# Kernel tuning notes

Hardware: AMD Instinct MI355X
Metric: run time of the kernel (lower is better)

The kernel has to match this reference:

```python
import jax, jax.numpy as jnp
import numpy as np

N = 10000          # num nodes
E = 640000         # num edges (avg degree 64)
IN_CH = 128
OUT_CH = 128


def setup_inputs() -> dict:
    key = jax.random.key(0)
    k_x, k_ei, k_ea, k_w1, k_b1, k_w2, k_b2 = jax.random.split(key, 7)
    x = jax.random.normal(k_x, (N, IN_CH), dtype=jnp.float32)
    edge_index = jax.random.randint(k_ei, (2, E), 0, N, dtype=jnp.int64)
    edge_attr = jax.random.uniform(k_ea, (E,), dtype=jnp.float32)
    # MLP params: Linear(2*in, out) -> ReLU -> Linear(out, out), stored as [in, out]
    s1 = 1.0 / np.sqrt(2 * IN_CH)
    s2 = 1.0 / np.sqrt(OUT_CH)
    W1 = jax.random.uniform(k_w1, (2 * IN_CH, OUT_CH), jnp.float32, -s1, s1)
    b1 = jax.random.uniform(k_b1, (OUT_CH,), jnp.float32, -s1, s1)
    W2 = jax.random.uniform(k_w2, (OUT_CH, OUT_CH), jnp.float32, -s2, s2)
    b2 = jax.random.uniform(k_b2, (OUT_CH,), jnp.float32, -s2, s2)
    return {"x": x, "edge_index": edge_index, "edge_attr": edge_attr,
            "W1": W1, "b1": b1, "W2": W2, "b2": b2}


def reference(x, edge_index, edge_attr, W1, b1, W2, b2):
    row, col = edge_index[0], edge_index[1]
    # message: scale sender feature by edge_attr, concat with receiver feature, 2-layer MLP
    x_i = x[row] * edge_attr[:, None]          # [E, in]
    x_j = x[col]                               # [E, in]
    combined = jnp.concatenate([x_i, x_j], axis=1)  # [E, 2*in]
    h = jax.nn.relu(combined @ W1 + b1)        # [E, out]
    messages = h @ W2 + b2                     # [E, out]
    # sum aggregation: scatter-add messages into receiving nodes (col)
    out = jnp.zeros((x.shape[0], messages.shape[1]), dtype=messages.dtype)
    out = out.at[col].add(messages)
    return out
```

## Files before the change

kernel.cpp:

```cpp
#include <hip/hip_runtime.h>

#define C 128
#define NPB 16
#define CAP 128
#define OVF_MAX 65536
#define CSTRIDE 16
#define EPT 8

__device__ __forceinline__ unsigned bf16_bits(float x) {
    unsigned u = __float_as_uint(x);
    u += 0x7FFFu + ((u >> 16) & 1u);
    return u >> 16;
}
__device__ __forceinline__ float bf16f(unsigned short b) {
    return __uint_as_float(((unsigned)b) << 16);
}

__global__ void fused_pre_kernel(const float* __restrict__ x, const float* __restrict__ W1,
                                 unsigned short* __restrict__ P16, float* __restrict__ Q,
                                 const int* __restrict__ ei, const float* __restrict__ attr,
                                 int* __restrict__ cursor, int* __restrict__ ovf_cnt,
                                 int2* __restrict__ ovf, unsigned* __restrict__ sorted,
                                 int N, int E, int SB) {
    if ((int)blockIdx.x < SB) {
        const int base = (blockIdx.x * 256 + threadIdx.x) * EPT;
        if (base >= E) return;
        if (base + EPT <= E) {
            const int4 r0 = *(const int4*)(ei + base);
            const int4 r1 = *(const int4*)(ei + base + 4);
            const int4 c0 = *(const int4*)(ei + (size_t)E + base);
            const int4 c1 = *(const int4*)(ei + (size_t)E + base + 4);
            const float4 a0 = *(const float4*)(attr + base);
            const float4 a1 = *(const float4*)(attr + base + 4);
            const int rows[EPT] = {r0.x, r0.y, r0.z, r0.w, r1.x, r1.y, r1.z, r1.w};
            const int cols[EPT] = {c0.x, c0.y, c0.z, c0.w, c1.x, c1.y, c1.z, c1.w};
            const float as[EPT] = {a0.x, a0.y, a0.z, a0.w, a1.x, a1.y, a1.z, a1.w};
            int pos[EPT];
#pragma unroll
            for (int j = 0; j < EPT; ++j)
                pos[j] = atomicAdd(&cursor[cols[j] * CSTRIDE], 1);
#pragma unroll
            for (int j = 0; j < EPT; ++j) {
                const unsigned v = (bf16_bits(as[j]) << 16) | (unsigned)rows[j];
                if (pos[j] < CAP) {
                    sorted[(size_t)cols[j] * CAP + pos[j]] = v;
                } else {
                    const int o = atomicAdd(ovf_cnt, 1);
                    if (o < OVF_MAX) ovf[o] = make_int2(cols[j], (int)v);
                }
            }
        } else {
            for (int e = base; e < E; ++e) {
                const int row = ei[e], colv = ei[(size_t)E + e];
                const int pos = atomicAdd(&cursor[colv * CSTRIDE], 1);
                const unsigned v = (bf16_bits(attr[e]) << 16) | (unsigned)row;
                if (pos < CAP) sorted[(size_t)colv * CAP + pos] = v;
                else {
                    const int o = atomicAdd(ovf_cnt, 1);
                    if (o < OVF_MAX) ovf[o] = make_int2(colv, (int)v);
                }
            }
        }
    } else {
        __shared__ float xs[NPB][C];
        const int pb = blockIdx.x - SB;
        const int n0 = pb * NPB;
        const int tt = threadIdx.x & (C - 1);
        const int half = threadIdx.x >> 7;
        for (int i = threadIdx.x; i < NPB * C; i += 256) {
            const int gi = n0 * C + i;
            xs[0][i] = (gi < N * C) ? x[gi] : 0.f;
        }
        __syncthreads();
        const float* __restrict__ Wb = W1 + (half ? (C * C) : 0) + tt;
        float acc[NPB] = {};
        for (int k = 0; k < C; ++k) {
            const float w = Wb[k * C];
#pragma unroll
            for (int j = 0; j < NPB; ++j)
                acc[j] = fmaf(xs[j][k], w, acc[j]);
        }
#pragma unroll
        for (int j = 0; j < NPB; ++j)
            if (n0 + j < N) {
                if (half) Q[(size_t)(n0 + j) * C + tt] = acc[j];
                else      P16[(size_t)(n0 + j) * C + tt] = (unsigned short)bf16_bits(acc[j]);
            }
    }
}

__global__ void agg_out_kernel(const unsigned* __restrict__ sorted, const int* __restrict__ cursor,
                               const unsigned short* __restrict__ P16, const float* __restrict__ Q,
                               const float* __restrict__ b1, const float* __restrict__ W2,
                               const float* __restrict__ b2,
                               const int* __restrict__ ovf_cnt, const int2* __restrict__ ovf,
                               float* __restrict__ out, int N) {
    __shared__ float4 part[2][4][32];
    __shared__ float hs[2][C];
    const int t = threadIdx.x;
    const int j = t >> 7;
    const int slice = (t >> 5) & 3;
    const int ch4 = t & 31;
    const int n = blockIdx.x * 2 + j;

    float4 acc = make_float4(0.f, 0.f, 0.f, 0.f);
    float4 qb = acc;
    int deg = 0;
    if (n < N) {
        deg = cursor[n * CSTRIDE];
        const float4 q4  = *(const float4*)(Q + (size_t)n * C + (ch4 << 2));
        const float4 b14 = *(const float4*)(b1 + (ch4 << 2));
        qb = make_float4(q4.x + b14.x, q4.y + b14.y, q4.z + b14.z, q4.w + b14.w);
        const int cnt = min(deg, CAP);
        const unsigned* __restrict__ buf = sorted + (size_t)n * CAP;
        const int chunk = (cnt + 3) >> 2;
        const int s0 = min(slice * chunk, cnt);
        const int s1 = min(s0 + chunk, cnt);
        int i = s0;
        for (; i + 4 <= s1; i += 4) {
            const unsigned v0 = buf[i], v1 = buf[i + 1], v2 = buf[i + 2], v3 = buf[i + 3];
            const ushort4 p0 = *(const ushort4*)(P16 + (((size_t)(v0 & 0xFFFFu)) << 7) + (ch4 << 2));
            const ushort4 p1 = *(const ushort4*)(P16 + (((size_t)(v1 & 0xFFFFu)) << 7) + (ch4 << 2));
            const ushort4 p2 = *(const ushort4*)(P16 + (((size_t)(v2 & 0xFFFFu)) << 7) + (ch4 << 2));
            const ushort4 p3 = *(const ushort4*)(P16 + (((size_t)(v3 & 0xFFFFu)) << 7) + (ch4 << 2));
            const float a0 = __uint_as_float(v0 & 0xFFFF0000u);
            const float a1 = __uint_as_float(v1 & 0xFFFF0000u);
            const float a2 = __uint_as_float(v2 & 0xFFFF0000u);
            const float a3 = __uint_as_float(v3 & 0xFFFF0000u);
            acc.x += fmaxf(fmaf(a0, bf16f(p0.x), qb.x), 0.f) + fmaxf(fmaf(a1, bf16f(p1.x), qb.x), 0.f)
                   + fmaxf(fmaf(a2, bf16f(p2.x), qb.x), 0.f) + fmaxf(fmaf(a3, bf16f(p3.x), qb.x), 0.f);
            acc.y += fmaxf(fmaf(a0, bf16f(p0.y), qb.y), 0.f) + fmaxf(fmaf(a1, bf16f(p1.y), qb.y), 0.f)
                   + fmaxf(fmaf(a2, bf16f(p2.y), qb.y), 0.f) + fmaxf(fmaf(a3, bf16f(p3.y), qb.y), 0.f);
            acc.z += fmaxf(fmaf(a0, bf16f(p0.z), qb.z), 0.f) + fmaxf(fmaf(a1, bf16f(p1.z), qb.z), 0.f)
                   + fmaxf(fmaf(a2, bf16f(p2.z), qb.z), 0.f) + fmaxf(fmaf(a3, bf16f(p3.z), qb.z), 0.f);
            acc.w += fmaxf(fmaf(a0, bf16f(p0.w), qb.w), 0.f) + fmaxf(fmaf(a1, bf16f(p1.w), qb.w), 0.f)
                   + fmaxf(fmaf(a2, bf16f(p2.w), qb.w), 0.f) + fmaxf(fmaf(a3, bf16f(p3.w), qb.w), 0.f);
        }
        for (; i < s1; ++i) {
            const unsigned v = buf[i];
            const ushort4 p = *(const ushort4*)(P16 + (((size_t)(v & 0xFFFFu)) << 7) + (ch4 << 2));
            const float a = __uint_as_float(v & 0xFFFF0000u);
            acc.x += fmaxf(fmaf(a, bf16f(p.x), qb.x), 0.f);
            acc.y += fmaxf(fmaf(a, bf16f(p.y), qb.y), 0.f);
            acc.z += fmaxf(fmaf(a, bf16f(p.z), qb.z), 0.f);
            acc.w += fmaxf(fmaf(a, bf16f(p.w), qb.w), 0.f);
        }
        if (slice == 0) {
            const int oc = min(*ovf_cnt, OVF_MAX);
            for (int o = 0; o < oc; ++o) {
                const int2 v = ovf[o];
                if (v.x == n) {
                    const unsigned u = (unsigned)v.y;
                    const ushort4 p = *(const ushort4*)(P16 + (((size_t)(u & 0xFFFFu)) << 7) + (ch4 << 2));
                    const float a = __uint_as_float(u & 0xFFFF0000u);
                    acc.x += fmaxf(fmaf(a, bf16f(p.x), qb.x), 0.f);
                    acc.y += fmaxf(fmaf(a, bf16f(p.y), qb.y), 0.f);
                    acc.z += fmaxf(fmaf(a, bf16f(p.z), qb.z), 0.f);
                    acc.w += fmaxf(fmaf(a, bf16f(p.w), qb.w), 0.f);
                }
            }
        }
    }
    part[j][slice][ch4] = acc;
    __syncthreads();
    if (slice == 0 && n < N) {
        const float4 r0 = part[j][0][ch4], r1 = part[j][1][ch4];
        const float4 r2 = part[j][2][ch4], r3 = part[j][3][ch4];
        float4 h;
        h.x = r0.x + r1.x + r2.x + r3.x;
        h.y = r0.y + r1.y + r2.y + r3.y;
        h.z = r0.z + r1.z + r2.z + r3.z;
        h.w = r0.w + r1.w + r2.w + r3.w;
        *(float4*)(&hs[j][ch4 << 2]) = h;
    }
    __syncthreads();
    float4 o = make_float4(0.f, 0.f, 0.f, 0.f);
    if (n < N) {
        const int k0 = slice << 5;
#pragma unroll 8
        for (int k = k0; k < k0 + 32; ++k) {
            const float hv = hs[j][k];
            const float4 w = *(const float4*)(W2 + (size_t)k * C + (ch4 << 2));
            o.x = fmaf(hv, w.x, o.x);
            o.y = fmaf(hv, w.y, o.y);
            o.z = fmaf(hv, w.z, o.z);
            o.w = fmaf(hv, w.w, o.w);
        }
    }
    __syncthreads();
    part[j][slice][ch4] = o;
    __syncthreads();
    if (slice == 0 && n < N) {
        const float4 r0 = part[j][0][ch4], r1 = part[j][1][ch4];
        const float4 r2 = part[j][2][ch4], r3 = part[j][3][ch4];
        const float4 b24 = *(const float4*)(b2 + (ch4 << 2));
        const float d = (float)deg;
        float4 res;
        res.x = fmaf(d, b24.x, r0.x + r1.x + r2.x + r3.x);
        res.y = fmaf(d, b24.y, r0.y + r1.y + r2.y + r3.y);
        res.z = fmaf(d, b24.z, r0.z + r1.z + r2.z + r3.z);
        res.w = fmaf(d, b24.w, r0.w + r1.w + r2.w + r3.w);
        *(float4*)(out + (size_t)n * C + (ch4 << 2)) = res;
    }
}

extern "C" void kernel_launch(void* const* d_in, const int* in_sizes, int n_in,
                              void* d_out, int out_size, void* d_ws, size_t ws_size,
                              hipStream_t stream) {
    const float* x    = (const float*)d_in[0];
    const int*   ei   = (const int*)d_in[1];
    const float* attr = (const float*)d_in[2];
    const float* W1   = (const float*)d_in[3];
    const float* b1   = (const float*)d_in[4];
    const float* W2   = (const float*)d_in[5];
    const float* b2   = (const float*)d_in[6];
    float* out = (float*)d_out;

    const int N = in_sizes[0] / C;
    const int E = in_sizes[2];

    char* ws = (char*)d_ws;
    unsigned short* P16 = (unsigned short*)ws;  ws += (size_t)N * C * sizeof(unsigned short);
    ws = (char*)(((uintptr_t)ws + 15) & ~(uintptr_t)15);
    float*    Q       = (float*)ws;     ws += (size_t)N * C * sizeof(float);
    unsigned* sorted  = (unsigned*)ws;  ws += (size_t)N * CAP * sizeof(unsigned);
    int2*     ovf     = (int2*)ws;      ws += (size_t)OVF_MAX * sizeof(int2);
    int*      cursor  = (int*)ws;       ws += (size_t)N * CSTRIDE * sizeof(int);
    int*      ovf_cnt = (int*)ws;

    hipMemsetAsync(cursor, 0, ((size_t)N * CSTRIDE + 1) * sizeof(int), stream);

    const int SB = (E + 256 * EPT - 1) / (256 * EPT);
    const int PB = (N + NPB - 1) / NPB;
    fused_pre_kernel<<<SB + PB, 256, 0, stream>>>(x, W1, P16, Q, ei, attr,
                                                  cursor, ovf_cnt, ovf, sorted, N, E, SB);
    agg_out_kernel<<<(N + 1) / 2, 256, 0, stream>>>(sorted, cursor, P16, Q, b1, W2, b2,
                                                    ovf_cnt, ovf, out, N);
}
```

Measured before the change: 157.9 us.

## Replace per-node global atomic bucketing with two-pass coarse bin sort

Edge bucketing by destination becomes a two-level counting sort. Each block first builds a shared-memory histogram over coarse bins of 32 nodes, reserves space per bin with one global atomic, and writes the edges into those bins. A new kernel then distributes each bin into per-node slots using shared-memory atomics. This removes the per-edge global atomics on strided cursors. The cost is an extra kernel launch, an intermediate 8-byte-per-edge buffer, and padding entries, and the degree count now adds the overflow edges.

```diff
diff --git a/kernel.cpp b/kernel.cpp
--- a/kernel.cpp
+++ b/kernel.cpp
@@ -4,8 +4,11 @@
 #define NPB 16
 #define CAP 128
 #define OVF_MAX 65536
-#define CSTRIDE 16
-#define EPT 8
+#define EPT1 16
+#define GSH 5
+#define G (1 << GSH)
+#define CAPB 3072
+#define MAXBIN 512
 
 __device__ __forceinline__ unsigned bf16_bits(float x) {
     unsigned u = __float_as_uint(x);
@@ -19,51 +22,83 @@
 __global__ void fused_pre_kernel(const float* __restrict__ x, const float* __restrict__ W1,
                                  unsigned short* __restrict__ P16, float* __restrict__ Q,
                                  const int* __restrict__ ei, const float* __restrict__ attr,
-                                 int* __restrict__ cursor, int* __restrict__ ovf_cnt,
-                                 int2* __restrict__ ovf, unsigned* __restrict__ sorted,
-                                 int N, int E, int SB) {
-    if ((int)blockIdx.x < SB) {
-        const int base = (blockIdx.x * 256 + threadIdx.x) * EPT;
-        if (base >= E) return;
-        if (base + EPT <= E) {
-            const int4 r0 = *(const int4*)(ei + base);
-            const int4 r1 = *(const int4*)(ei + base + 4);
-            const int4 c0 = *(const int4*)(ei + (size_t)E + base);
-            const int4 c1 = *(const int4*)(ei + (size_t)E + base + 4);
-            const float4 a0 = *(const float4*)(attr + base);
-            const float4 a1 = *(const float4*)(attr + base + 4);
-            const int rows[EPT] = {r0.x, r0.y, r0.z, r0.w, r1.x, r1.y, r1.z, r1.w};
-            const int cols[EPT] = {c0.x, c0.y, c0.z, c0.w, c1.x, c1.y, c1.z, c1.w};
-            const float as[EPT] = {a0.x, a0.y, a0.z, a0.w, a1.x, a1.y, a1.z, a1.w};
-            int pos[EPT];
-#pragma unroll
-            for (int j = 0; j < EPT; ++j)
-                pos[j] = atomicAdd(&cursor[cols[j] * CSTRIDE], 1);
-#pragma unroll
-            for (int j = 0; j < EPT; ++j) {
-                const unsigned v = (bf16_bits(as[j]) << 16) | (unsigned)rows[j];
-                if (pos[j] < CAP) {
-                    sorted[(size_t)cols[j] * CAP + pos[j]] = v;
+                                 uint2* __restrict__ bins, int* __restrict__ bin_cursor,
+                                 int* __restrict__ ovf_cnt, int2* __restrict__ ovf,
+                                 int N, int E, int PBLK, int NBIN) {
+    if ((int)blockIdx.x < PBLK) {
+        __shared__ int hist[MAXBIN];
+        __shared__ int boff[MAXBIN];
+        for (int i = threadIdx.x; i < NBIN; i += 256) { hist[i] = 0; boff[i] = 0; }
+        __syncthreads();
+        const int base = ((int)blockIdx.x * 256 + (int)threadIdx.x) * EPT1;
+        const int rem = (base < E) ? min(EPT1, E - base) : 0;
+        const bool vec = (rem == EPT1) && ((E & 3) == 0);
+        if (vec) {
+#pragma unroll
+            for (int j0 = 0; j0 < EPT1; j0 += 4) {
+                const int4 c = *(const int4*)(ei + (size_t)E + base + j0);
+                atomicAdd(&hist[c.x >> GSH], 1);
+                atomicAdd(&hist[c.y >> GSH], 1);
+                atomicAdd(&hist[c.z >> GSH], 1);
+                atomicAdd(&hist[c.w >> GSH], 1);
+            }
+        } else {
+            for (int j = 0; j < rem; ++j)
+                atomicAdd(&hist[ei[(size_t)E + base + j] >> GSH], 1);
+        }
+        __syncthreads();
+        for (int i = threadIdx.x; i < NBIN; i += 256) {
+            const int c = hist[i];
+            int b = 0;
+            if (c) {
+                const int cp = (c + 7) & ~7;
+                b = atomicAdd(&bin_cursor[i], cp);
+                for (int k = c; k < cp; ++k)
+                    if (b + k < CAPB)
+                        bins[(size_t)i * CAPB + b + k] = make_uint2(0u, 0xFFFFFFFFu);
+            }
+            hist[i] = b;
+        }
+        __syncthreads();
+        if (vec) {
+#pragma unroll
+            for (int j0 = 0; j0 < EPT1; j0 += 4) {
+                const int4 r = *(const int4*)(ei + base + j0);
+                const int4 c = *(const int4*)(ei + (size_t)E + base + j0);
+                const float4 a = *(const float4*)(attr + base + j0);
+                const int rr[4] = {r.x, r.y, r.z, r.w};
+                const int cc[4] = {c.x, c.y, c.z, c.w};
+                const float aa[4] = {a.x, a.y, a.z, a.w};
+#pragma unroll
+                for (int j = 0; j < 4; ++j) {
+                    const int bin = cc[j] >> GSH;
+                    const int idx = hist[bin] + atomicAdd(&boff[bin], 1);
+                    const unsigned pk = (bf16_bits(aa[j]) << 16) | (unsigned)rr[j];
+                    if (idx < CAPB) {
+                        bins[(size_t)bin * CAPB + idx] = make_uint2(pk, (unsigned)cc[j]);
+                    } else {
+                        const int o = atomicAdd(ovf_cnt, 1);
+                        if (o < OVF_MAX) ovf[o] = make_int2(cc[j], (int)pk);
+                    }
+                }
+            }
+        } else {
+            for (int j = 0; j < rem; ++j) {
+                const int row = ei[base + j], colv = ei[(size_t)E + base + j];
+                const int bin = colv >> GSH;
+                const int idx = hist[bin] + atomicAdd(&boff[bin], 1);
+                const unsigned pk = (bf16_bits(attr[base + j]) << 16) | (unsigned)row;
+                if (idx < CAPB) {
+                    bins[(size_t)bin * CAPB + idx] = make_uint2(pk, (unsigned)colv);
                 } else {
                     const int o = atomicAdd(ovf_cnt, 1);
-                    if (o < OVF_MAX) ovf[o] = make_int2(cols[j], (int)v);
-                }
-            }
-        } else {
-            for (int e = base; e < E; ++e) {
-                const int row = ei[e], colv = ei[(size_t)E + e];
-                const int pos = atomicAdd(&cursor[colv * CSTRIDE], 1);
-                const unsigned v = (bf16_bits(attr[e]) << 16) | (unsigned)row;
-                if (pos < CAP) sorted[(size_t)colv * CAP + pos] = v;
-                else {
-                    const int o = atomicAdd(ovf_cnt, 1);
-                    if (o < OVF_MAX) ovf[o] = make_int2(colv, (int)v);
+                    if (o < OVF_MAX) ovf[o] = make_int2(colv, (int)pk);
                 }
             }
         }
     } else {
         __shared__ float xs[NPB][C];
-        const int pb = blockIdx.x - SB;
+        const int pb = (int)blockIdx.x - PBLK;
         const int n0 = pb * NPB;
         const int tt = threadIdx.x & (C - 1);
         const int half = threadIdx.x >> 7;
@@ -87,6 +122,34 @@
                 else      P16[(size_t)(n0 + j) * C + tt] = (unsigned short)bf16_bits(acc[j]);
             }
     }
+}
+
+__global__ void bin_scatter_kernel(const uint2* __restrict__ bins, const int* __restrict__ bin_cursor,
+                                   unsigned* __restrict__ sorted, int* __restrict__ cursor,
+                                   int* __restrict__ ovf_cnt, int2* __restrict__ ovf, int N) {
+    __shared__ int off[G];
+    const int b = blockIdx.x;
+    const int n0 = b << GSH;
+    if (threadIdx.x < G) off[threadIdx.x] = 0;
+    __syncthreads();
+    const int cnt = min(bin_cursor[b], CAPB);
+    const uint2* __restrict__ src = bins + (size_t)b * CAPB;
+    for (int i = threadIdx.x; i < cnt; i += 256) {
+        const uint2 e = src[i];
+        const unsigned noff = e.y - (unsigned)n0;
+        if (noff < (unsigned)G) {
+            const int pos = atomicAdd(&off[noff], 1);
+            if (pos < CAP) {
+                sorted[(size_t)e.y * CAP + pos] = e.x;
+            } else {
+                const int o = atomicAdd(ovf_cnt, 1);
+                if (o < OVF_MAX) ovf[o] = make_int2((int)e.y, (int)e.x);
+            }
+        }
+    }
+    __syncthreads();
+    if (threadIdx.x < G && n0 + (int)threadIdx.x < N)
+        cursor[n0 + threadIdx.x] = min(off[threadIdx.x], CAP);
 }
 
 __global__ void agg_out_kernel(const unsigned* __restrict__ sorted, const int* __restrict__ cursor,
@@ -106,8 +169,9 @@
     float4 acc = make_float4(0.f, 0.f, 0.f, 0.f);
     float4 qb = acc;
     int deg = 0;
+    int mcnt = 0;
     if (n < N) {
-        deg = cursor[n * CSTRIDE];
+        deg = cursor[n];
         const float4 q4  = *(const float4*)(Q + (size_t)n * C + (ch4 << 2));
         const float4 b14 = *(const float4*)(b1 + (ch4 << 2));
         qb = make_float4(q4.x + b14.x, q4.y + b14.y, q4.z + b14.z, q4.w + b14.w);
@@ -150,6 +214,7 @@
             for (int o = 0; o < oc; ++o) {
                 const int2 v = ovf[o];
                 if (v.x == n) {
+                    ++mcnt;
                     const unsigned u = (unsigned)v.y;
                     const ushort4 p = *(const ushort4*)(P16 + (((size_t)(u & 0xFFFFu)) << 7) + (ch4 << 2));
                     const float a = __uint_as_float(u & 0xFFFF0000u);
@@ -194,7 +259,7 @@
         const float4 r0 = part[j][0][ch4], r1 = part[j][1][ch4];
         const float4 r2 = part[j][2][ch4], r3 = part[j][3][ch4];
         const float4 b24 = *(const float4*)(b2 + (ch4 << 2));
-        const float d = (float)deg;
+        const float d = (float)(deg + mcnt);
         float4 res;
         res.x = fmaf(d, b24.x, r0.x + r1.x + r2.x + r3.x);
         res.y = fmaf(d, b24.y, r0.y + r1.y + r2.y + r3.y);
@@ -218,22 +283,28 @@
 
     const int N = in_sizes[0] / C;
     const int E = in_sizes[2];
+    const int NBIN = (N + G - 1) >> GSH;
 
     char* ws = (char*)d_ws;
     unsigned short* P16 = (unsigned short*)ws;  ws += (size_t)N * C * sizeof(unsigned short);
     ws = (char*)(((uintptr_t)ws + 15) & ~(uintptr_t)15);
     float*    Q       = (float*)ws;     ws += (size_t)N * C * sizeof(float);
     unsigned* sorted  = (unsigned*)ws;  ws += (size_t)N * CAP * sizeof(unsigned);
+    uint2*    bins    = (uint2*)ws;     ws += (size_t)NBIN * CAPB * sizeof(uint2);
     int2*     ovf     = (int2*)ws;      ws += (size_t)OVF_MAX * sizeof(int2);
-    int*      cursor  = (int*)ws;       ws += (size_t)N * CSTRIDE * sizeof(int);
+    int*      cursor  = (int*)ws;       ws += (size_t)N * sizeof(int);
+    int*      bin_cursor = (int*)ws;    ws += (size_t)NBIN * sizeof(int);
     int*      ovf_cnt = (int*)ws;
 
-    hipMemsetAsync(cursor, 0, ((size_t)N * CSTRIDE + 1) * sizeof(int), stream);
-
-    const int SB = (E + 256 * EPT - 1) / (256 * EPT);
+    hipMemsetAsync(bin_cursor, 0, ((size_t)NBIN + 1) * sizeof(int), stream);
+
+    const int PBLK = (E + 256 * EPT1 - 1) / (256 * EPT1);
     const int PB = (N + NPB - 1) / NPB;
-    fused_pre_kernel<<<SB + PB, 256, 0, stream>>>(x, W1, P16, Q, ei, attr,
-                                                  cursor, ovf_cnt, ovf, sorted, N, E, SB);
+    fused_pre_kernel<<<PBLK + PB, 256, 0, stream>>>(x, W1, P16, Q, ei, attr,
+                                                    bins, bin_cursor, ovf_cnt, ovf,
+                                                    N, E, PBLK, NBIN);
+    bin_scatter_kernel<<<NBIN, 256, 0, stream>>>(bins, bin_cursor, sorted, cursor,
+                                                 ovf_cnt, ovf, N);
     agg_out_kernel<<<(N + 1) / 2, 256, 0, stream>>>(sorted, cursor, P16, Q, b1, W2, b2,
                                                     ovf_cnt, ovf, out, N);
 }
```

New measurement: 143.0 us. -9.5%, faster.
